# Kernel tuning notes

Hardware: AMD Instinct MI355X
Metric: run time of the kernel (lower is better)

## Reference

```python
import jax, jax.numpy as jnp
import numpy as np

DIM = 512      # model dim
HEADS = 8      # attention heads
WS = 256       # window_size
G = 32         # num_global_tokens
SPARSITY = 0.3 # fraction of entries masked out per row by the sparsity controller


def setup_inputs() -> dict:
    key = jax.random.key(0)
    ks = jax.random.split(key, 7)
    b, n = 4, 8192
    x = jax.random.normal(ks[0], (b, n, DIM), dtype=jnp.float32)
    w_qkv = jax.random.normal(ks[1], (DIM, 3 * DIM), dtype=jnp.float32) * (DIM ** -0.5)
    w_out = jax.random.normal(ks[2], (DIM, DIM), dtype=jnp.float32) * (DIM ** -0.5)
    b_out = jnp.zeros((DIM,), dtype=jnp.float32)
    local_bias = jax.random.normal(ks[3], (HEADS, WS, WS), dtype=jnp.float32)
    global_param = jax.random.normal(ks[4], (HEADS, G, WS), dtype=jnp.float32)
    gate = jax.random.normal(ks[5], (HEADS,), dtype=jnp.float32)
    return {"x": x, "w_qkv": w_qkv, "w_out": w_out, "b_out": b_out,
            "local_bias": local_bias, "global_param": global_param, "gate": gate}


def reference(x, w_qkv, w_out, b_out, local_bias, global_param, gate):
    b, n, _ = x.shape
    h, ws, g = HEADS, WS, G
    d = DIM // h
    w = n // ws  # number of windows
    scale = DIM ** -0.5

    qkv = x @ w_qkv                      # [b, n, 3*dim]
    q, k, v = jnp.split(qkv, 3, axis=-1)

    def to_win(t):  # [b, n, dim] -> [b, h, w, ws, d]
        return t.reshape(b, n, h, d).transpose(0, 2, 1, 3).reshape(b, h, w, ws, d)

    q, k, v = to_win(q), to_win(k), to_win(v)

    # windowed local attention with learned per-window additive bias
    local = jnp.einsum('bhwnd,bhwmd->bhwnm', q, k) * scale   # [b,h,w,ws,ws]
    local = local + local_bias[None, :, None]                # bias broadcast over b, w

    # global-token attention term built from window-averaged q/k
    q_mean = q.mean(axis=2)  # [b,h,ws,d]
    k_mean = k.mean(axis=2)  # [b,h,ws,d]
    global_q = jnp.einsum('hgn,bhnd->bhgd', global_param, q_mean)      # [b,h,g,d]
    global_scores = jnp.einsum('bhgd,bhmd->bhgm', global_q, k_mean) * scale  # [b,h,g,ws]
    global_bias = global_scores.mean(axis=2)                            # [b,h,ws]

    # sparsity controller: learned per-head gate combines local + global,
    # then top-k row sparsification keeps (1-sparsity) of entries pre-softmax
    gate_h = jax.nn.sigmoid(gate)[None, :, None, None, None]
    scores = local + gate_h * global_bias[:, :, None, None, :]          # [b,h,w,ws,ws]
    k_keep = int(ws * (1.0 - SPARSITY))
    thresh = jax.lax.top_k(scores, k_keep)[0][..., -1:]                 # kth largest per row
    scores = jnp.where(scores >= thresh, scores, jnp.float32(-1e9))

    attn = jax.nn.softmax(scores, axis=-1)
    out = jnp.einsum('bhwnm,bhwmd->bhwnd', attn, v)                     # [b,h,w,ws,d]
    out = out.reshape(b, h, n, d).transpose(0, 2, 1, 3).reshape(b, n, DIM)
    return out @ w_out + b_out
```

## Files before the change

### kernel.cpp

```cpp
#include <hip/hip_runtime.h>

#define NN    8192
#define WSZ   256
#define KKEEP 179
#define SCALE 0.044194173824159216f

typedef __attribute__((ext_vector_type(8))) __bf16 bf16x8;
typedef __attribute__((ext_vector_type(4))) short  s16x4;
typedef __attribute__((ext_vector_type(8))) short  s16x8;
typedef __attribute__((ext_vector_type(4))) float  f32x4;

struct Split3 { short h, m, l; };
__device__ __forceinline__ Split3 split3(float x)
{
    unsigned u  = __float_as_uint(x);
    unsigned hb = ((u + 0x7FFFu + ((u >> 16) & 1u)) >> 16) << 16;
    float r = x - __uint_as_float(hb);
    unsigned ur = __float_as_uint(r);
    unsigned mb = ((ur + 0x7FFFu + ((ur >> 16) & 1u)) >> 16) << 16;
    float r2 = r - __uint_as_float(mb);
    unsigned lr = __float_as_uint(r2);
    unsigned lb = (lr + 0x7FFFu + ((lr >> 16) & 1u)) >> 16;
    Split3 s;
    s.h = (short)(hb >> 16);
    s.m = (short)(mb >> 16);
    s.l = (short)(lb & 0xFFFFu);
    return s;
}

__device__ __forceinline__ void split2(float x, short& h, short& m)
{
    unsigned u  = __float_as_uint(x);
    unsigned hb = ((u + 0x7FFFu + ((u >> 16) & 1u)) >> 16) << 16;
    float r = x - __uint_as_float(hb);
    unsigned ur = __float_as_uint(r);
    unsigned mb = (ur + 0x7FFFu + ((ur >> 16) & 1u)) >> 16;
    h = (short)(hb >> 16);
    m = (short)(mb & 0xFFFFu);
}

__global__ __launch_bounds__(256) void splitw_kernel(const float* __restrict__ W,
                                                     int K, int N,
                                                     short* __restrict__ h,
                                                     short* __restrict__ m,
                                                     short* __restrict__ l)
{
    int idx = blockIdx.x * 256 + threadIdx.x;
    if (idx >= K * N) return;
    int k = idx / N, n = idx - k * N;
    Split3 s = split3(W[idx]);
    size_t o = (size_t)n * K + k;
    h[o] = s.h; m[o] = s.m; l[o] = s.l;
}

__global__ __launch_bounds__(256, 2) void gemm_mfma(const float* __restrict__ A, int lda,
                                                    const short* __restrict__ BTh,
                                                    const short* __restrict__ BTm,
                                                    const short* __restrict__ BTl,
                                                    const float* __restrict__ bias,
                                                    float* __restrict__ C, int ldc,
                                                    int qk_cols)
{
    __shared__ __align__(16) short Asm[3][128 * 40];
    __shared__ __align__(16) short Bsm[3][128 * 40];

    const int t       = threadIdx.x;
    const int lane    = t & 63;
    const int wave    = t >> 6;
    const int wr      = wave >> 1;
    const int wc      = wave & 1;
    const int rowBase = blockIdx.y * 128;
    const int colBase = blockIdx.x * 128;
    const int pstart  = (colBase < qk_cols) ? 0 : 3;

    const int sa[6] = {2, 0, 1, 1, 0, 0};
    const int sb[6] = {0, 2, 1, 0, 1, 0};

    const int fn = lane & 15;
    const int fq = (lane >> 4) * 8;

    f32x4 acc[4][4] = {};

    for (int ks = 0; ks < 512; ks += 32) {
        __syncthreads();

#pragma unroll
        for (int lo = 0; lo < 4; ++lo) {
            int idx = lo * 256 + t;
            int am  = idx >> 3;
            int af  = (idx & 7) * 4;
            float4 a4 = *(const float4*)&A[(size_t)(rowBase + am) * lda + ks + af];
            Split3 s0 = split3(a4.x);
            Split3 s1 = split3(a4.y);
            Split3 s2 = split3(a4.z);
            Split3 s3 = split3(a4.w);
            s16x4 hv, mv, lv;
            hv[0] = s0.h; hv[1] = s1.h; hv[2] = s2.h; hv[3] = s3.h;
            mv[0] = s0.m; mv[1] = s1.m; mv[2] = s2.m; mv[3] = s3.m;
            lv[0] = s0.l; lv[1] = s1.l; lv[2] = s2.l; lv[3] = s3.l;
            int o = am * 40 + af;
            *(s16x4*)&Asm[0][o] = hv;
            *(s16x4*)&Asm[1][o] = mv;
            *(s16x4*)&Asm[2][o] = lv;
        }
#pragma unroll
        for (int lo = 0; lo < 2; ++lo) {
            int c = lo * 256 + t;
            int n = c >> 2;
            int q = (c & 3) * 8;
            size_t src = (size_t)(colBase + n) * 512 + ks + q;
            int o = n * 40 + q;
            *(s16x8*)&Bsm[0][o] = *(const s16x8*)&BTh[src];
            *(s16x8*)&Bsm[1][o] = *(const s16x8*)&BTm[src];
            *(s16x8*)&Bsm[2][o] = *(const s16x8*)&BTl[src];
        }
        __syncthreads();

        bf16x8 Bf[3][4];
#pragma unroll
        for (int s = 0; s < 3; ++s)
#pragma unroll
            for (int j = 0; j < 4; ++j)
                Bf[s][j] = *(const bf16x8*)&Bsm[s][(wc * 64 + j * 16 + fn) * 40 + fq];

#pragma unroll
        for (int i = 0; i < 4; ++i) {
            bf16x8 Af[3];
#pragma unroll
            for (int s = 0; s < 3; ++s)
                Af[s] = *(const bf16x8*)&Asm[s][(wr * 64 + i * 16 + fn) * 40 + fq];
#pragma unroll
            for (int p = 0; p < 6; ++p) {
                if (p < pstart) continue;
#pragma unroll
                for (int j = 0; j < 4; ++j)
                    acc[i][j] = __builtin_amdgcn_mfma_f32_16x16x32_bf16(
                        Af[sa[p]], Bf[sb[p]][j], acc[i][j], 0, 0, 0);
            }
        }
    }

    const int crow0 = rowBase + wr * 64 + (lane >> 4) * 4;
    const int ccol0 = colBase + wc * 64 + fn;
#pragma unroll
    for (int j = 0; j < 4; ++j) {
        int col = ccol0 + j * 16;
        float bv = bias ? bias[col] : 0.0f;
#pragma unroll
        for (int i = 0; i < 4; ++i)
#pragma unroll
            for (int r = 0; r < 4; ++r)
                C[(size_t)(crow0 + i * 16 + r) * ldc + col] = acc[i][j][r] + bv;
    }
}

__global__ __launch_bounds__(256) void means_kernel(const float* __restrict__ qkv,
                                                    float* __restrict__ q_mean,
                                                    float* __restrict__ k_mean)
{
    int idx = blockIdx.x * 256 + threadIdx.x;
    int dd = idx & 63;
    int i  = (idx >> 6) & 255;
    int bh = idx >> 14;
    int b = bh >> 3, h = bh & 7;
    const float* base = qkv + (size_t)b * NN * 1536 + (size_t)h * 64 + dd;
    float qs = 0.f, ks = 0.f;
#pragma unroll
    for (int w = 0; w < 32; ++w) {
        size_t off = (size_t)(w * 256 + i) * 1536;
        qs += base[off];
        ks += base[off + 512];
    }
    q_mean[idx] = qs * 0.03125f;
    k_mean[idx] = ks * 0.03125f;
}

__global__ __launch_bounds__(256) void globalbias_kernel(const float* __restrict__ q_mean,
                                                         const float* __restrict__ k_mean,
                                                         const float* __restrict__ gp,
                                                         float* __restrict__ gbias)
{
    __shared__ float gq[32 * 64];
    const int bh = blockIdx.x;
    const int h  = bh & 7;
    const int t  = threadIdx.x;

#pragma unroll
    for (int e = 0; e < 8; ++e) {
        int idx = e * 256 + t;
        int g  = idx >> 6;
        int dd = idx & 63;
        const float* gpr = gp + (size_t)(h * 32 + g) * 256;
        const float* qm  = q_mean + (size_t)bh * 16384 + dd;
        float s = 0.f;
        for (int i = 0; i < 256; ++i) s += gpr[i] * qm[(size_t)i * 64];
        gq[idx] = s;
    }
    __syncthreads();

    const float* km = k_mean + (size_t)bh * 16384 + (size_t)t * 64;
    float4 kr[16];
#pragma unroll
    for (int j = 0; j < 16; ++j) kr[j] = *(const float4*)&km[4 * j];
    float acc = 0.f;
    for (int g = 0; g < 32; ++g) {
        const float* gqr = &gq[g * 64];
        float s = 0.f;
#pragma unroll
        for (int j = 0; j < 16; ++j) {
            float4 q4 = *(const float4*)&gqr[4 * j];
            s += q4.x * kr[j].x + q4.y * kr[j].y + q4.z * kr[j].z + q4.w * kr[j].w;
        }
        acc += s;
    }
    gbias[bh * 256 + t] = acc * SCALE * 0.03125f;
}

__device__ __forceinline__ unsigned mono_enc(float f) {
    unsigned u = __float_as_uint(f);
    return (u & 0x80000000u) ? ~u : (u | 0x80000000u);
}
__device__ __forceinline__ float mono_dec(unsigned e) {
    return (e & 0x80000000u) ? __uint_as_float(e ^ 0x80000000u)
                             : __uint_as_float(~e);
}

__global__ __launch_bounds__(256, 3) void attn_kernel(float* __restrict__ qkv,
                                                      const float* __restrict__ local_bias,
                                                      const float* __restrict__ gbias,
                                                      const float* __restrict__ gate)
{
    __shared__ __align__(16) short Qs[3 * 64 * 64];
    __shared__ __align__(16) short Ks[3 * 64 * 64];
    float* st = (float*)(void*)Ks;

    const int t    = threadIdx.x;
    const int lane = t & 63;
    const int wave = t >> 6;
    const int wr   = wave >> 1;
    const int wc   = wave & 1;
    const int fn   = lane & 15;
    const int fq   = (lane >> 4) * 8;
    const int g4   = (lane >> 4) * 4;

    const int blk = blockIdx.x;
    const int rc  = blk & 3;
    const int w   = (blk >> 2) & 31;
    const int bh  = blk >> 7;
    const int h   = bh & 7;
    const int b   = bh >> 3;
    const float gateh = 1.0f / (1.0f + __expf(-gate[h]));

    const size_t tokBase = (size_t)b * NN + (size_t)w * WSZ;
    float* qb = qkv + tokBase * 1536 + h * 64;
    const float* kb = qb + 512;
    const float* vb = qb + 1024;

    const int rr = t >> 2, sub = t & 3;

    const int sa[6] = {2, 0, 1, 1, 0, 0};
    const int sb[6] = {0, 2, 1, 0, 1, 0};

#pragma unroll
    for (int l = 0; l < 4; ++l) {
        int f  = l * 256 + t;
        int r  = f >> 4;
        int dg = (f & 15) * 4;
        float4 a4 = *(const float4*)&qb[(size_t)(rc * 64 + r) * 1536 + dg];
        Split3 s0 = split3(a4.x), s1 = split3(a4.y), s2 = split3(a4.z), s3 = split3(a4.w);
        s16x4 hv, mv, lv;
        hv[0] = s0.h; hv[1] = s1.h; hv[2] = s2.h; hv[3] = s3.h;
        mv[0] = s0.m; mv[1] = s1.m; mv[2] = s2.m; mv[3] = s3.m;
        lv[0] = s0.l; lv[1] = s1.l; lv[2] = s2.l; lv[3] = s3.l;
        int o = r * 64 + (dg ^ ((r & 7) << 3));
        *(s16x4*)&Qs[o]        = hv;
        *(s16x4*)&Qs[4096 + o] = mv;
        *(s16x4*)&Qs[8192 + o] = lv;
    }

    float vals[64];
#pragma unroll
    for (int mc = 0; mc < 4; ++mc) {
        __syncthreads();
#pragma unroll
        for (int l = 0; l < 4; ++l) {
            int f  = l * 256 + t;
            int m  = f >> 4;
            int dg = (f & 15) * 4;
            float4 a4 = *(const float4*)&kb[(size_t)(mc * 64 + m) * 1536 + dg];
            Split3 s0 = split3(a4.x), s1 = split3(a4.y), s2 = split3(a4.z), s3 = split3(a4.w);
            s16x4 hv, mv, lv;
            hv[0] = s0.h; hv[1] = s1.h; hv[2] = s2.h; hv[3] = s3.h;
            mv[0] = s0.m; mv[1] = s1.m; mv[2] = s2.m; mv[3] = s3.m;
            lv[0] = s0.l; lv[1] = s1.l; lv[2] = s2.l; lv[3] = s3.l;
            int o = m * 64 + (dg ^ ((m & 7) << 3));
            *(s16x4*)&Ks[o]        = hv;
            *(s16x4*)&Ks[4096 + o] = mv;
            *(s16x4*)&Ks[8192 + o] = lv;
        }
        __syncthreads();

        f32x4 acc[2][2] = {};
#pragma unroll
        for (int kk = 0; kk < 2; ++kk) {
            bf16x8 Af[3][2], Bf[3][2];
#pragma unroll
            for (int s = 0; s < 3; ++s)
#pragma unroll
                for (int i = 0; i < 2; ++i) {
                    int ar = wr * 32 + i * 16 + fn;
                    int bc = wc * 32 + i * 16 + fn;
                    Af[s][i] = *(const bf16x8*)&Qs[s * 4096 + ar * 64 + ((kk * 32 + fq) ^ ((ar & 7) << 3))];
                    Bf[s][i] = *(const bf16x8*)&Ks[s * 4096 + bc * 64 + ((kk * 32 + fq) ^ ((bc & 7) << 3))];
                }
#pragma unroll
            for (int p = 0; p < 6; ++p)
#pragma unroll
                for (int i = 0; i < 2; ++i)
#pragma unroll
                    for (int j = 0; j < 2; ++j)
                        acc[i][j] = __builtin_amdgcn_mfma_f32_16x16x32_bf16(
                            Af[sa[p]][i], Bf[sb[p]][j], acc[i][j], 0, 0, 0);
        }
        __syncthreads();

#pragma unroll
        for (int j = 0; j < 2; ++j) {
            int cl = wc * 32 + j * 16 + fn;
            int cf = mc * 64 + cl;
            float gb = gateh * gbias[bh * 256 + cf];
#pragma unroll
            for (int i = 0; i < 2; ++i)
#pragma unroll
                for (int r = 0; r < 4; ++r) {
                    int rl = wr * 32 + i * 16 + g4 + r;
                    st[rl * 68 + cl] = acc[i][j][r] * SCALE
                        + local_bias[((size_t)h * 256 + rc * 64 + rl) * 256 + cf] + gb;
                }
        }
        __syncthreads();
#pragma unroll
        for (int j = 0; j < 16; ++j)
            vals[mc * 16 + j] = st[rr * 68 + sub + 4 * j];
    }

    float rmin = vals[0], rmax = vals[0];
#pragma unroll
    for (int j = 1; j < 64; ++j) {
        rmin = fminf(rmin, vals[j]);
        rmax = fmaxf(rmax, vals[j]);
    }
    rmin = fminf(rmin, __shfl_xor(rmin, 1)); rmin = fminf(rmin, __shfl_xor(rmin, 2));
    rmax = fmaxf(rmax, __shfl_xor(rmax, 1)); rmax = fmaxf(rmax, __shfl_xor(rmax, 2));

    float flo = rmin, fhi = rmax;
    float thr = 0.f;
    bool  done = false;
    for (int it = 0; it < 16; ++it) {
        if (__all(done ? 1 : 0)) break;
        float mf = 0.5f * (flo + fhi);
        int c = 0;
#pragma unroll
        for (int j = 0; j < 64; ++j) c += (vals[j] >= mf) ? 1 : 0;
        c += __shfl_xor(c, 1);
        c += __shfl_xor(c, 2);
        if (!done) {
            if (c == KKEEP)      { thr = mf; done = true; }
            else if (c > KKEEP)  flo = mf;
            else                 fhi = mf;
        }
    }
    if (__any(done ? 0 : 1)) {
        unsigned lo_u = mono_enc(flo), hi_u = mono_enc(fhi);
        for (int it = 0; it < 34; ++it) {
            bool active = (!done) && (lo_u < hi_u);
            if (!__any(active ? 1 : 0)) break;
            unsigned span = hi_u - lo_u;
            unsigned mid  = lo_u + (span >> 1) + (span & 1u);
            float mf = mono_dec(mid);
            int c = 0;
#pragma unroll
            for (int j = 0; j < 64; ++j) c += (vals[j] >= mf) ? 1 : 0;
            c += __shfl_xor(c, 1);
            c += __shfl_xor(c, 2);
            if (active) {
                if (c == KKEEP)      { thr = mf; done = true; }
                else if (c >= KKEEP) lo_u = mid;
                else                 hi_u = mid - 1;
            }
        }
        if (!done) thr = mono_dec(lo_u);
    }

    float rmx = -3e38f;
#pragma unroll
    for (int j = 0; j < 64; ++j) rmx = fmaxf(rmx, (vals[j] >= thr) ? vals[j] : -3e38f);
    rmx = fmaxf(rmx, __shfl_xor(rmx, 1));
    rmx = fmaxf(rmx, __shfl_xor(rmx, 2));
    float rsum = 0.f;
#pragma unroll
    for (int j = 0; j < 64; ++j) {
        float e = (vals[j] >= thr) ? __expf(vals[j] - rmx) : 0.f;
        vals[j] = e;
        rsum += e;
    }
    rsum += __shfl_xor(rsum, 1);
    rsum += __shfl_xor(rsum, 2);
    float rinv = 1.0f / rsum;
#pragma unroll
    for (int j = 0; j < 64; ++j) vals[j] *= rinv;

    const int sa2[3] = {1, 0, 0};
    const int sb2[3] = {0, 1, 0};
    f32x4 acc2[2][2] = {};
#pragma unroll
    for (int mc = 0; mc < 4; ++mc) {
        __syncthreads();
#pragma unroll
        for (int u = 0; u < 16; ++u) {
            short ph, pm;
            split2(vals[mc * 16 + u], ph, pm);
            int ml   = sub + 4 * u;
            int slot = rr * 64 + (ml ^ ((rr & 7) << 3));
            Qs[slot]        = ph;
            Qs[4096 + slot] = pm;
        }
#pragma unroll
        for (int l = 0; l < 2; ++l) {
            int f  = l * 256 + t;
            int d  = f & 63;
            int mo = (f >> 6) * 8;
            s16x8 hv, mv;
#pragma unroll
            for (int i = 0; i < 8; ++i) {
                short vh, vm;
                split2(vb[(size_t)(mc * 64 + mo + i) * 1536 + d], vh, vm);
                hv[i] = vh; mv[i] = vm;
            }
            int o = d * 72 + mo;
            *(s16x8*)&Ks[o]        = hv;
            *(s16x8*)&Ks[4608 + o] = mv;
        }
        __syncthreads();

#pragma unroll
        for (int kk = 0; kk < 2; ++kk) {
            bf16x8 Pf[2][2], Vf[2][2];
#pragma unroll
            for (int s = 0; s < 2; ++s)
#pragma unroll
                for (int i = 0; i < 2; ++i) {
                    int pr = wr * 32 + i * 16 + fn;
                    int dr = wc * 32 + i * 16 + fn;
                    Pf[s][i] = *(const bf16x8*)&Qs[s * 4096 + pr * 64 + ((kk * 32 + fq) ^ ((pr & 7) << 3))];
                    Vf[s][i] = *(const bf16x8*)&Ks[s * 4608 + dr * 72 + kk * 32 + fq];
                }
#pragma unroll
            for (int p = 0; p < 3; ++p)
#pragma unroll
                for (int i = 0; i < 2; ++i)
#pragma unroll
                    for (int j = 0; j < 2; ++j)
                        acc2[i][j] = __builtin_amdgcn_mfma_f32_16x16x32_bf16(
                            Pf[sa2[p]][i], Vf[sb2[p]][j], acc2[i][j], 0, 0, 0);
        }
    }

#pragma unroll
    for (int j = 0; j < 2; ++j)
#pragma unroll
        for (int i = 0; i < 2; ++i)
#pragma unroll
            for (int r = 0; r < 4; ++r) {
                int row = rc * 64 + wr * 32 + i * 16 + g4 + r;
                int d   = wc * 32 + j * 16 + fn;
                qb[(size_t)row * 1536 + d] = acc2[i][j][r];
            }
}

extern "C" void kernel_launch(void* const* d_in, const int* in_sizes, int n_in,
                              void* d_out, int out_size, void* d_ws, size_t ws_size,
                              hipStream_t stream)
{
    (void)in_sizes; (void)n_in; (void)out_size; (void)ws_size;
    const float* x            = (const float*)d_in[0];
    const float* w_qkv        = (const float*)d_in[1];
    const float* w_out        = (const float*)d_in[2];
    const float* b_out        = (const float*)d_in[3];
    const float* local_bias   = (const float*)d_in[4];
    const float* global_param = (const float*)d_in[5];
    const float* gate         = (const float*)d_in[6];
    float* out = (float*)d_out;
    float* ws  = (float*)d_ws;

    float* qkv    = ws;
    float* q_mean = qkv + (size_t)32768 * 1536;
    float* k_mean = q_mean + (size_t)32 * 256 * 64;
    float* gb     = k_mean + (size_t)32 * 256 * 64;
    short* wsp    = (short*)(gb + 8192);
    short* WTh  = wsp;
    short* WTm  = WTh + (size_t)1536 * 512;
    short* WTl  = WTm + (size_t)1536 * 512;
    short* WoTh = WTl + (size_t)1536 * 512;
    short* WoTm = WoTh + (size_t)512 * 512;
    short* WoTl = WoTm + (size_t)512 * 512;

    splitw_kernel<<<3072, 256, 0, stream>>>(w_qkv, 512, 1536, WTh, WTm, WTl);
    splitw_kernel<<<1024, 256, 0, stream>>>(w_out, 512, 512, WoTh, WoTm, WoTl);
    gemm_mfma<<<dim3(12, 256), 256, 0, stream>>>(x, 512, WTh, WTm, WTl,
                                                 nullptr, qkv, 1536, 1024);
    means_kernel<<<2048, 256, 0, stream>>>(qkv, q_mean, k_mean);
    globalbias_kernel<<<32, 256, 0, stream>>>(q_mean, k_mean, global_param, gb);
    attn_kernel<<<4096, 256, 0, stream>>>(qkv, local_bias, gb, gate);
    gemm_mfma<<<dim3(4, 256), 256, 0, stream>>>(qkv, 1536, WoTh, WoTm, WoTl,
                                                b_out, out, 512, 0);
}
```

Baseline: 740.3 us.

## Pre-split QKV GEMM operands into swizzled tiles and load via global_load_lds

Adds a pre-pass that splits x and w_qkv into bf16 hi/mid/lo planes stored as pre-tiled, XOR-swizzled 128x32 blocks. A new GEMM kernel then copies those tiles straight into LDS with async global_load_lds, so the main loop no longer does per-tile fp32 splitting or register staging. The fallback GEMM also switches from padded to XOR-swizzled LDS and raises its occupancy hint to 3. The new path needs a larger workspace and writes and re-reads about 100 MB of split activations, in exchange for a simpler GEMM inner loop.

Result: faster. 692.0 us, median of 2 (-6.5%).

```diff
diff --git a/kernel.cpp b/kernel.cpp
--- a/kernel.cpp
+++ b/kernel.cpp
@@ -4,6 +4,9 @@
 #define WSZ   256
 #define KKEEP 179
 #define SCALE 0.044194173824159216f
+
+#define APLANE ((size_t)32768 * 512)
+#define BPLANE ((size_t)1536 * 512)
 
 typedef __attribute__((ext_vector_type(8))) __bf16 bf16x8;
 typedef __attribute__((ext_vector_type(4))) short  s16x4;
@@ -39,6 +42,13 @@
     m = (short)(mb & 0xFFFFu);
 }
 
+__device__ __forceinline__ void async_copy16(short* dst_lds, const short* src)
+{
+    __builtin_amdgcn_global_load_lds(
+        (const __attribute__((address_space(1))) void*)src,
+        (__attribute__((address_space(3))) void*)dst_lds, 16, 0, 0);
+}
+
 __global__ __launch_bounds__(256) void splitw_kernel(const float* __restrict__ W,
                                                      int K, int N,
                                                      short* __restrict__ h,
@@ -53,7 +63,151 @@
     h[o] = s.h; m[o] = s.m; l[o] = s.l;
 }
 
-__global__ __launch_bounds__(256, 2) void gemm_mfma(const float* __restrict__ A, int lda,
+__global__ __launch_bounds__(256) void splitw_tiled(const float* __restrict__ W, int N,
+                                                    short* __restrict__ Bh,
+                                                    short* __restrict__ Bm,
+                                                    short* __restrict__ Bl)
+{
+    __shared__ float raw[32 * 128];
+    const int cb = blockIdx.x >> 4;
+    const int kt = blockIdx.x & 15;
+    const int t  = threadIdx.x;
+
+#pragma unroll
+    for (int l = 0; l < 4; ++l) {
+        int f  = l * 256 + t;
+        int k  = f >> 5;
+        int nf = (f & 31) * 4;
+        *(float4*)&raw[k * 128 + nf] =
+            *(const float4*)&W[(size_t)(kt * 32 + k) * N + cb * 128 + nf];
+    }
+    __syncthreads();
+
+    const int r  = t >> 1;
+    const int hf = t & 1;
+    const size_t base = ((size_t)(cb * 16 + kt) * 128 + r) * 32;
+#pragma unroll
+    for (int ss = 0; ss < 2; ++ss) {
+        int s2 = hf * 2 + ss;
+        s16x8 hv, mv, lv;
+#pragma unroll
+        for (int j = 0; j < 8; ++j) {
+            Split3 sp = split3(raw[(s2 * 8 + j) * 128 + r]);
+            hv[j] = sp.h; mv[j] = sp.m; lv[j] = sp.l;
+        }
+        size_t o = base + (size_t)((s2 ^ ((r >> 1) & 3)) << 3);
+        *(s16x8*)&Bh[o] = hv;
+        *(s16x8*)&Bm[o] = mv;
+        *(s16x8*)&Bl[o] = lv;
+    }
+}
+
+__global__ __launch_bounds__(256) void splitA_kernel(const float* __restrict__ X,
+                                                     short* __restrict__ Ah,
+                                                     short* __restrict__ Am,
+                                                     short* __restrict__ Al)
+{
+    int idx = blockIdx.x * 256 + threadIdx.x;
+    int row = idx >> 7;
+    int kf  = (idx & 127) << 2;
+    float4 a4 = *(const float4*)&X[((size_t)row << 9) + kf];
+    int rb = row >> 7, r = row & 127;
+    int kt = kf >> 5;
+    int s  = (kf >> 3) & 3;
+    int jj = kf & 7;
+    size_t o = ((size_t)(rb * 16 + kt) * 128 + r) * 32
+             + (size_t)((s ^ ((r >> 1) & 3)) << 3) + jj;
+    Split3 s0 = split3(a4.x), s1 = split3(a4.y), s2 = split3(a4.z), s3 = split3(a4.w);
+    s16x4 hv, mv, lv;
+    hv[0] = s0.h; hv[1] = s1.h; hv[2] = s2.h; hv[3] = s3.h;
+    mv[0] = s0.m; mv[1] = s1.m; mv[2] = s2.m; mv[3] = s3.m;
+    lv[0] = s0.l; lv[1] = s1.l; lv[2] = s2.l; lv[3] = s3.l;
+    *(s16x4*)&Ah[o] = hv;
+    *(s16x4*)&Am[o] = mv;
+    *(s16x4*)&Al[o] = lv;
+}
+
+__global__ __launch_bounds__(256, 3) void gemm_gload(const short* __restrict__ Ab,
+                                                     const short* __restrict__ Bb,
+                                                     float* __restrict__ C)
+{
+    __shared__ __align__(16) short S[6 * 4096];
+
+    const int t    = threadIdx.x;
+    const int lane = t & 63;
+    const int wave = t >> 6;
+    const int wr   = wave >> 1;
+    const int wc   = wave & 1;
+    const int fn   = lane & 15;
+    const int slot = lane >> 4;
+    const int rowBlk = blockIdx.y;
+    const int colBlk = blockIdx.x;
+    const int pstart = (colBlk < 8) ? 0 : 3;
+
+    const int sa[6] = {2, 0, 1, 1, 0, 0};
+    const int sb[6] = {0, 2, 1, 0, 1, 0};
+
+    f32x4 acc[4][4] = {};
+
+    for (int kt = 0; kt < 16; ++kt) {
+        __syncthreads();
+        const short* aT = Ab + ((size_t)(rowBlk * 16 + kt) << 12);
+        const short* bT = Bb + ((size_t)(colBlk * 16 + kt) << 12);
+#pragma unroll
+        for (int c = 0; c < 12; ++c) {
+            int g = wave * 12 + c;
+            int p = g >> 3;
+            int q = g & 7;
+            const short* src = (p < 3 ? aT + (size_t)p * APLANE
+                                      : bT + (size_t)(p - 3) * BPLANE)
+                             + q * 512 + lane * 8;
+            async_copy16(&S[g * 512], src);
+        }
+        __syncthreads();
+
+        bf16x8 Bf[3][4];
+#pragma unroll
+        for (int s = 0; s < 3; ++s)
+#pragma unroll
+            for (int j = 0; j < 4; ++j) {
+                int rowb = wc * 64 + j * 16 + fn;
+                Bf[s][j] = *(const bf16x8*)&S[(3 + s) * 4096 + rowb * 32
+                                              + ((slot ^ ((rowb >> 1) & 3)) << 3)];
+            }
+
+#pragma unroll
+        for (int i = 0; i < 4; ++i) {
+            int rowa = wr * 64 + i * 16 + fn;
+            bf16x8 Af[3];
+#pragma unroll
+            for (int s = 0; s < 3; ++s)
+                Af[s] = *(const bf16x8*)&S[s * 4096 + rowa * 32
+                                           + ((slot ^ ((rowa >> 1) & 3)) << 3)];
+#pragma unroll
+            for (int p = 0; p < 6; ++p) {
+                if (p < pstart) continue;
+#pragma unroll
+                for (int j = 0; j < 4; ++j)
+                    acc[i][j] = __builtin_amdgcn_mfma_f32_16x16x32_bf16(
+                        Af[sa[p]], Bf[sb[p]][j], acc[i][j], 0, 0, 0);
+            }
+        }
+    }
+
+    const int crow0 = rowBlk * 128 + wr * 64 + (lane >> 4) * 4;
+    const int ccol0 = colBlk * 128 + wc * 64 + fn;
+#pragma unroll
+    for (int j = 0; j < 4; ++j) {
+        int col = ccol0 + j * 16;
+#pragma unroll
+        for (int i = 0; i < 4; ++i)
+#pragma unroll
+            for (int r = 0; r < 4; ++r)
+                C[(size_t)(crow0 + i * 16 + r) * 1536 + col] = acc[i][j][r];
+    }
+}
+
+__global__ __launch_bounds__(256, 3) void gemm_mfma(const float* __restrict__ A, int lda,
                                                     const short* __restrict__ BTh,
                                                     const short* __restrict__ BTm,
                                                     const short* __restrict__ BTl,
@@ -61,8 +215,8 @@
                                                     float* __restrict__ C, int ldc,
                                                     int qk_cols)
 {
-    __shared__ __align__(16) short Asm[3][128 * 40];
-    __shared__ __align__(16) short Bsm[3][128 * 40];
+    __shared__ __align__(16) short Asm[3][128 * 32];
+    __shared__ __align__(16) short Bsm[3][128 * 32];
 
     const int t       = threadIdx.x;
     const int lane    = t & 63;
@@ -76,8 +230,8 @@
     const int sa[6] = {2, 0, 1, 1, 0, 0};
     const int sb[6] = {0, 2, 1, 0, 1, 0};
 
-    const int fn = lane & 15;
-    const int fq = (lane >> 4) * 8;
+    const int fn   = lane & 15;
+    const int slot = lane >> 4;
 
     f32x4 acc[4][4] = {};
 
@@ -98,7 +252,7 @@
             hv[0] = s0.h; hv[1] = s1.h; hv[2] = s2.h; hv[3] = s3.h;
             mv[0] = s0.m; mv[1] = s1.m; mv[2] = s2.m; mv[3] = s3.m;
             lv[0] = s0.l; lv[1] = s1.l; lv[2] = s2.l; lv[3] = s3.l;
-            int o = am * 40 + af;
+            int o = am * 32 + (((af >> 3) ^ ((am >> 1) & 3)) << 3) + (af & 4);
             *(s16x4*)&Asm[0][o] = hv;
             *(s16x4*)&Asm[1][o] = mv;
             *(s16x4*)&Asm[2][o] = lv;
@@ -109,7 +263,7 @@
             int n = c >> 2;
             int q = (c & 3) * 8;
             size_t src = (size_t)(colBase + n) * 512 + ks + q;
-            int o = n * 40 + q;
+            int o = n * 32 + (((q >> 3) ^ ((n >> 1) & 3)) << 3);
             *(s16x8*)&Bsm[0][o] = *(const s16x8*)&BTh[src];
             *(s16x8*)&Bsm[1][o] = *(const s16x8*)&BTm[src];
             *(s16x8*)&Bsm[2][o] = *(const s16x8*)&BTl[src];
@@ -120,15 +274,20 @@
 #pragma unroll
         for (int s = 0; s < 3; ++s)
 #pragma unroll
-            for (int j = 0; j < 4; ++j)
-                Bf[s][j] = *(const bf16x8*)&Bsm[s][(wc * 64 + j * 16 + fn) * 40 + fq];
+            for (int j = 0; j < 4; ++j) {
+                int rowb = wc * 64 + j * 16 + fn;
+                Bf[s][j] = *(const bf16x8*)&Bsm[s][rowb * 32
+                                                   + ((slot ^ ((rowb >> 1) & 3)) << 3)];
+            }
 
 #pragma unroll
         for (int i = 0; i < 4; ++i) {
+            int rowa = wr * 64 + i * 16 + fn;
             bf16x8 Af[3];
 #pragma unroll
             for (int s = 0; s < 3; ++s)
-                Af[s] = *(const bf16x8*)&Asm[s][(wr * 64 + i * 16 + fn) * 40 + fq];
+                Af[s] = *(const bf16x8*)&Asm[s][rowa * 32
+                                                + ((slot ^ ((rowa >> 1) & 3)) << 3)];
 #pragma unroll
             for (int p = 0; p < 6; ++p) {
                 if (p < pstart) continue;
@@ -482,7 +641,7 @@
                               void* d_out, int out_size, void* d_ws, size_t ws_size,
                               hipStream_t stream)
 {
-    (void)in_sizes; (void)n_in; (void)out_size; (void)ws_size;
+    (void)in_sizes; (void)n_in; (void)out_size;
     const float* x            = (const float*)d_in[0];
     const float* w_qkv        = (const float*)d_in[1];
     const float* w_out        = (const float*)d_in[2];
@@ -498,17 +657,30 @@
     float* k_mean = q_mean + (size_t)32 * 256 * 64;
     float* gb     = k_mean + (size_t)32 * 256 * 64;
     short* wsp    = (short*)(gb + 8192);
-    short* WTh  = wsp;
-    short* WTm  = WTh + (size_t)1536 * 512;
-    short* WTl  = WTm + (size_t)1536 * 512;
-    short* WoTh = WTl + (size_t)1536 * 512;
+    short* WoTh = wsp;
     short* WoTm = WoTh + (size_t)512 * 512;
     short* WoTl = WoTm + (size_t)512 * 512;
-
-    splitw_kernel<<<3072, 256, 0, stream>>>(w_qkv, 512, 1536, WTh, WTm, WTl);
+    short* WqB  = WoTl + (size_t)512 * 512;
+    short* Almb = WqB + 3 * BPLANE;
+
+    size_t need = (size_t)((char*)(Almb + 3 * APLANE) - (char*)ws);
+    bool pre = ws_size >= need;
+
     splitw_kernel<<<1024, 256, 0, stream>>>(w_out, 512, 512, WoTh, WoTm, WoTl);
-    gemm_mfma<<<dim3(12, 256), 256, 0, stream>>>(x, 512, WTh, WTm, WTl,
-                                                 nullptr, qkv, 1536, 1024);
+
+    if (pre) {
+        splitw_tiled<<<192, 256, 0, stream>>>(w_qkv, 1536,
+                                              WqB, WqB + BPLANE, WqB + 2 * BPLANE);
+        splitA_kernel<<<16384, 256, 0, stream>>>(x, Almb, Almb + APLANE, Almb + 2 * APLANE);
+        gemm_gload<<<dim3(12, 256), 256, 0, stream>>>(Almb, WqB, qkv);
+    } else {
+        splitw_kernel<<<3072, 256, 0, stream>>>(w_qkv, 512, 1536,
+                                                WqB, WqB + BPLANE, WqB + 2 * BPLANE);
+        gemm_mfma<<<dim3(12, 256), 256, 0, stream>>>(x, 512, WqB, WqB + BPLANE,
+                                                     WqB + 2 * BPLANE,
+                                                     nullptr, qkv, 1536, 1024);
+    }
+
     means_kernel<<<2048, 256, 0, stream>>>(qkv, q_mean, k_mean);
     globalbias_kernel<<<32, 256, 0, stream>>>(q_mean, k_mean, global_param, gb);
     attn_kernel<<<4096, 256, 0, stream>>>(qkv, local_bias, gb, gate);
```
